# Kernel tuning notes

Hardware: AMD Instinct MI355X
Metric: run time of the kernel (lower is better)

Reference implementation:

```python
import jax, jax.numpy as jnp
import numpy as np

B, S, D = 4, 4096, 1024

def setup_inputs() -> dict:
    key = jax.random.key(0)
    k0, k1, k2, k3 = jax.random.split(key, 4)
    x = jax.random.normal(k0, (B, S, D), dtype=jnp.float32)
    # nn.Linear weights, applied as x @ W.T; init scaled ~1/sqrt(D)
    Wq = jax.random.normal(k1, (D, D), dtype=jnp.float32) / np.sqrt(D)
    Wk = jax.random.normal(k2, (D, D), dtype=jnp.float32) / np.sqrt(D)
    Wv = jax.random.normal(k3, (D, D), dtype=jnp.float32) / np.sqrt(D)
    return {"x": x, "Wq": Wq, "Wk": Wk, "Wv": Wv}

def reference(x, Wq, Wk, Wv):
    scale = x.shape[-1] ** (-0.5)
    Q = jnp.einsum('bsd,ed->bse', x, Wq)  # nn.Linear: x @ W.T
    K = jnp.einsum('bsd,ed->bse', x, Wk)
    V = jnp.einsum('bsd,ed->bse', x, Wv)
    scores = jax.nn.softmax(jnp.einsum('bqd,bkd->bqk', Q, K) * scale, axis=-1)
    return jnp.einsum('bqk,bkd->bqd', scores, V)
```

## Files before the change

### kernel.cpp

```cpp
#include <hip/hip_runtime.h>

typedef __bf16 bf16_t;
typedef bf16_t bf16x8 __attribute__((ext_vector_type(8)));
typedef float floatx4 __attribute__((ext_vector_type(4)));
typedef int i32x4 __attribute__((ext_vector_type(4)));

#define VMCNT(n) asm volatile("s_waitcnt vmcnt(" #n ")" ::: "memory")
#define LGKM(n)  asm volatile("s_waitcnt lgkmcnt(" #n ")" ::: "memory")
#define SCHED0   __builtin_amdgcn_sched_barrier(0)
#define DSR(dst, base, off) \
  asm volatile("ds_read_b128 %0, %1 offset:" #off : "=v"(dst) : "v"(base))

__device__ __forceinline__ void wg_barrier() {
  asm volatile("" ::: "memory");
  __builtin_amdgcn_s_barrier();
  asm volatile("" ::: "memory");
}

__device__ __forceinline__ void async_load16(const bf16_t* g, bf16_t* l) {
  __builtin_amdgcn_global_load_lds(
      (const __attribute__((address_space(1))) unsigned int*)g,
      (__attribute__((address_space(3))) unsigned int*)l, 16, 0, 0);
}

__device__ __forceinline__ unsigned lds_addr(const bf16_t* p) {
  return (unsigned)(unsigned long long)
      (__attribute__((address_space(3))) const bf16_t*)p;
}

__device__ __forceinline__ int xcd_swizzle(int p, int total) {
  return (total % 8 == 0) ? (p & 7) * (total >> 3) + (p >> 3) : p;
}

__device__ __forceinline__ void mfma16(
    floatx4 (&a4)[4][2],
    i32x4 x0, i32x4 x1, i32x4 x2, i32x4 x3,
    i32x4 x4, i32x4 x5, i32x4 x6, i32x4 x7,
    i32x4 y0, i32x4 y1, i32x4 y2, i32x4 y3)
{
  const bf16x8 A0[4] = {__builtin_bit_cast(bf16x8, x0), __builtin_bit_cast(bf16x8, x1),
                        __builtin_bit_cast(bf16x8, x2), __builtin_bit_cast(bf16x8, x3)};
  const bf16x8 A1[4] = {__builtin_bit_cast(bf16x8, x4), __builtin_bit_cast(bf16x8, x5),
                        __builtin_bit_cast(bf16x8, x6), __builtin_bit_cast(bf16x8, x7)};
  const bf16x8 B0[2] = {__builtin_bit_cast(bf16x8, y0), __builtin_bit_cast(bf16x8, y1)};
  const bf16x8 B1[2] = {__builtin_bit_cast(bf16x8, y2), __builtin_bit_cast(bf16x8, y3)};
  #pragma unroll
  for (int i = 0; i < 4; ++i)
    #pragma unroll
    for (int j = 0; j < 2; ++j) {
      a4[i][j] = __builtin_amdgcn_mfma_f32_16x16x32_bf16(A0[i], B0[j], a4[i][j], 0, 0, 0);
      a4[i][j] = __builtin_amdgcn_mfma_f32_16x16x32_bf16(A1[i], B1[j], a4[i][j], 0, 0, 0);
    }
}

__device__ __forceinline__ void gemm_acc256(
    const bf16_t* __restrict__ A, const bf16_t* __restrict__ B,
    int K, int lda, int ldb, int bm, int bn, floatx4 (&acc)[4][4][2])
{
  __shared__ bf16_t lA[2][16384];
  __shared__ bf16_t lB[2][16384];
  const int t = threadIdx.x;
  const int lane = t & 63;
  const int w = t >> 6;
  const int wm64 = (w & 1) * 64;
  const int wn32 = (w >> 1) * 32;
  const int fr = lane & 15;
  const int fk = ((lane >> 4) ^ ((fr >> 1) & 3)) * 8;

  const int r0 = t >> 2;
  const int ksw = ((t & 3) ^ ((r0 >> 1) & 3)) * 8;
  const long aRow = (long)(bm + r0) * lda + ksw;
  const long bRow = (long)(bn + r0) * ldb + ksw;
  const int NT = K >> 6;

  const unsigned baseA = lds_addr(&lA[0][0]);
  const unsigned baseB = lds_addr(&lB[0][0]);
  const unsigned fragA = baseA + (unsigned)(((wm64 + fr) * 32 + fk) * 2);
  const unsigned fragB = baseB + (unsigned)(((wn32 + fr) * 32 + fk) * 2);

  auto stageA = [&](int buf, int h, int u) {
    const bf16_t* s = A + aRow + (long)h * 128 * lda + u * 64;
    bf16_t* d = &lA[buf][h * 4096 + t * 8];
    async_load16(s, d);
    async_load16(s + 32, d + 8192);
  };
  auto stageB = [&](int buf, int h, int u) {
    const bf16_t* s = B + bRow + (long)h * 128 * ldb + u * 64;
    bf16_t* d = &lB[buf][h * 4096 + t * 8];
    async_load16(s, d);
    async_load16(s + 32, d + 8192);
  };

  stageA(0, 0, 0);
  stageB(0, 0, 0);
  stageB(0, 1, 0);
  stageA(0, 1, 0);
  stageA(1, 0, 1);
  stageB(1, 0, 1);
  VMCNT(8);
  wg_barrier();

  i32x4 al0,al1,al2,al3,al4,al5,al6,al7;
  i32x4 ah0,ah1,ah2,ah3,ah4,ah5,ah6,ah7;
  i32x4 vl0,vl1,vl2,vl3;
  i32x4 vh0,vh1,vh2,vh3;

  {
    const unsigned aC = fragA, bC = fragB;
    DSR(al0, aC, 0);     DSR(al1, aC, 1024);
    DSR(al2, aC, 2048);  DSR(al3, aC, 3072);
    DSR(al4, aC, 16384); DSR(al5, aC, 17408);
    DSR(al6, aC, 18432); DSR(al7, aC, 19456);
    DSR(vl0, bC, 0);     DSR(vl1, bC, 1024);
    DSR(vl2, bC, 16384); DSR(vl3, bC, 17408);
  }

  for (int u = 0; u < NT; ++u) {
    const int b = u & 1;
    const unsigned aC = fragA + (b ? 32768u : 0u);
    const unsigned bC = fragB + (b ? 32768u : 0u);
    const unsigned aN = fragA + (b ? 0u : 32768u);
    const unsigned bN = fragB + (b ? 0u : 32768u);

    if (u + 1 < NT) stageB(b ^ 1, 1, u + 1);
    if (u < NT - 1) { VMCNT(8); }
    DSR(vh0, bC, 8192);  DSR(vh1, bC, 9216);
    DSR(vh2, bC, 24576); DSR(vh3, bC, 25600);
    LGKM(4); SCHED0;
    __builtin_amdgcn_s_setprio(1);
    mfma16(acc[0], al0,al1,al2,al3,al4,al5,al6,al7, vl0,vl1,vl2,vl3);
    __builtin_amdgcn_s_setprio(0);
    wg_barrier();

    if (u + 1 < NT) stageA(b ^ 1, 1, u + 1);
    if (u < NT - 1) { VMCNT(8); }
    DSR(ah0, aC, 8192);  DSR(ah1, aC, 9216);
    DSR(ah2, aC, 10240); DSR(ah3, aC, 11264);
    DSR(ah4, aC, 24576); DSR(ah5, aC, 25600);
    DSR(ah6, aC, 26624); DSR(ah7, aC, 27648);
    LGKM(8); SCHED0;
    __builtin_amdgcn_s_setprio(1);
    mfma16(acc[1], al0,al1,al2,al3,al4,al5,al6,al7, vh0,vh1,vh2,vh3);
    __builtin_amdgcn_s_setprio(0);
    wg_barrier();

    if (u + 2 < NT) { stageA(b, 0, u + 2); VMCNT(8); }
    LGKM(0); SCHED0;
    __builtin_amdgcn_s_setprio(1);
    mfma16(acc[2], ah0,ah1,ah2,ah3,ah4,ah5,ah6,ah7, vl0,vl1,vl2,vl3);
    __builtin_amdgcn_s_setprio(0);
    wg_barrier();

    if (u + 2 < NT)       { stageB(b, 0, u + 2); VMCNT(8); }
    else if (u == NT - 2) { VMCNT(0); }
    if (u + 1 < NT) {
      DSR(al0, aN, 0);     DSR(al1, aN, 1024);
      DSR(al2, aN, 2048);  DSR(al3, aN, 3072);
      DSR(al4, aN, 16384); DSR(al5, aN, 17408);
      DSR(al6, aN, 18432); DSR(al7, aN, 19456);
      DSR(vl0, bN, 0);     DSR(vl1, bN, 1024);
      DSR(vl2, bN, 16384); DSR(vl3, bN, 17408);
    }
    __builtin_amdgcn_s_setprio(1);
    mfma16(acc[3], ah0,ah1,ah2,ah3,ah4,ah5,ah6,ah7, vh0,vh1,vh2,vh3);
    __builtin_amdgcn_s_setprio(0);
    wg_barrier();
  }
}

__device__ __forceinline__ void decode_grid(int& z, int& by, int& bx) {
  const int gx = gridDim.x, gy = gridDim.y;
  const int total = gx * gy * gridDim.z;
  int P = ((int)blockIdx.z * gy + (int)blockIdx.y) * gx + (int)blockIdx.x;
  int L = xcd_swizzle(P, total);
  z = L / (gx * gy);
  const int rem = L - z * gx * gy;
  if ((gx & 3) == 0 && (gy & 3) == 0) {
    const int sid = rem >> 4, w16 = rem & 15;
    const int spx = gx >> 2;
    const int sty = sid / spx, stx = sid - sty * spx;
    bx = stx * 4 + (w16 & 3);
    by = sty * 4 + (w16 >> 2);
  } else if ((gx & 3) == 0) {
    by = rem / gx; bx = rem - by * gx;
  } else {
    by = rem / gx; bx = rem - by * gx;
  }
}

__global__ __launch_bounds__(512, 2) void gemm_qkv(
    const bf16_t* __restrict__ xb, const bf16_t* __restrict__ Wqb,
    const bf16_t* __restrict__ Wkb, const bf16_t* __restrict__ Wvb,
    bf16_t* __restrict__ Q, bf16_t* __restrict__ Kp, bf16_t* __restrict__ Vt)
{
  const int L = xcd_swizzle((int)blockIdx.x, 768);
  const int z = L >> 8;
  const int r = L & 255;
  const bf16_t *A, *B; bf16_t* C;
  int bm, bn, ldc;
  if (z == 0)      { A = xb;  B = Wqb; C = Q;  bm = (r >> 2) * 256; bn = (r & 3) * 256; ldc = 1024; }
  else if (z == 1) { A = xb;  B = Wkb; C = Kp; bm = (r >> 2) * 256; bn = (r & 3) * 256; ldc = 1024; }
  else             { A = Wvb; B = xb;  C = Vt; bm = (r & 3) * 256; bn = (r >> 2) * 256; ldc = 16384; }
  floatx4 acc[4][4][2] = {};
  gemm_acc256(A, B, 1024, 1024, 1024, bm, bn, acc);

  const int t = threadIdx.x;
  const int lane = t & 63;
  const int w = t >> 6;
  const int wm64 = (w & 1) * 64;
  const int wn32 = (w >> 1) * 32;
  const int rq = (lane >> 4) * 4;
  const int c15 = lane & 15;
  #pragma unroll
  for (int q = 0; q < 4; ++q) {
    const int rB = bm + (q >> 1) * 128 + wm64;
    const int cB = bn + (q & 1) * 128 + wn32;
    #pragma unroll
    for (int i = 0; i < 4; ++i)
      #pragma unroll
      for (int j = 0; j < 2; ++j)
        #pragma unroll
        for (int r2 = 0; r2 < 4; ++r2)
          C[(long)(rB + i * 16 + rq + r2) * ldc + cB + j * 16 + c15] =
              (bf16_t)acc[q][i][j][r2];
  }
}

__global__ __launch_bounds__(512, 2) void gemm_qk_exp(
    const bf16_t* __restrict__ A, const bf16_t* __restrict__ B,
    bf16_t* __restrict__ C, float* __restrict__ rowsum,
    int K, int lda, int ldb, int ldc,
    long sA, long sB, long sC, long sR, float scale)
{
  __shared__ float rs[256];
  int z, by, bx;
  decode_grid(z, by, bx);
  A += (long)z * sA; B += (long)z * sB; C += (long)z * sC;
  rowsum += (long)z * sR;
  const int bm = by * 256, bn = bx * 256;
  if (threadIdx.x < 256) rs[threadIdx.x] = 0.f;
  floatx4 acc[4][4][2] = {};
  gemm_acc256(A, B, K, lda, ldb, bm, bn, acc);

  const int t = threadIdx.x;
  const int lane = t & 63;
  const int w = t >> 6;
  const int wm64 = (w & 1) * 64;
  const int wn32 = (w >> 1) * 32;
  const int rq = (lane >> 4) * 4;
  const int c15 = lane & 15;
  #pragma unroll
  for (int q = 0; q < 4; ++q) {
    const int rB = bm + (q >> 1) * 128 + wm64;
    const int cB = bn + (q & 1) * 128 + wn32;
    #pragma unroll
    for (int i = 0; i < 4; ++i) {
      #pragma unroll
      for (int r2 = 0; r2 < 4; ++r2) {
        const int row = rB + i * 16 + rq + r2;
        float psum = 0.f;
        #pragma unroll
        for (int j = 0; j < 2; ++j) {
          const float e = __expf(acc[q][i][j][r2] * scale);
          const bf16_t h = (bf16_t)e;
          C[(long)row * ldc + cB + j * 16 + c15] = h;
          psum += (float)h;
        }
        #pragma unroll
        for (int off = 8; off >= 1; off >>= 1)
          psum += __shfl_xor(psum, off, 16);
        if (c15 == 0) atomicAdd(&rs[row - bm], psum);
      }
    }
  }
  __syncthreads();
  if (t < 256) atomicAdd(&rowsum[bm + t], rs[t]);
}

__global__ __launch_bounds__(512, 2) void gemm_pv(
    const bf16_t* __restrict__ A, const bf16_t* __restrict__ B,
    float* __restrict__ C, const float* __restrict__ rowsum,
    int K, int lda, int ldb, int ldc,
    long sA, long sB, long sC, long sR)
{
  int z, by, bx;
  decode_grid(z, by, bx);
  A += (long)z * sA; B += (long)z * sB; C += (long)z * sC;
  rowsum += (long)z * sR;
  const int bm = by * 256, bn = bx * 256;
  floatx4 acc[4][4][2] = {};
  gemm_acc256(A, B, K, lda, ldb, bm, bn, acc);

  const int t = threadIdx.x;
  const int lane = t & 63;
  const int w = t >> 6;
  const int wm64 = (w & 1) * 64;
  const int wn32 = (w >> 1) * 32;
  const int rq = (lane >> 4) * 4;
  const int c15 = lane & 15;
  #pragma unroll
  for (int q = 0; q < 4; ++q) {
    const int rB = bm + (q >> 1) * 128 + wm64;
    const int cB = bn + (q & 1) * 128 + wn32;
    #pragma unroll
    for (int i = 0; i < 4; ++i) {
      #pragma unroll
      for (int r2 = 0; r2 < 4; ++r2) {
        const int row = rB + i * 16 + rq + r2;
        const float inv = 1.0f / rowsum[row];
        #pragma unroll
        for (int j = 0; j < 2; ++j)
          C[(long)row * ldc + cB + j * 16 + c15] = acc[q][i][j][r2] * inv;
      }
    }
  }
}

__global__ __launch_bounds__(256) void cvt_f32_bf16(
    const float* __restrict__ in, bf16_t* __restrict__ out, long n,
    float* __restrict__ rowsum, int nrs)
{
  const int bid = blockIdx.x;
  if (rowsum && bid < 64) {
    const int k = bid * 256 + threadIdx.x;
    if (k < nrs) rowsum[k] = 0.f;
  }
  long i = ((long)bid * 256 + threadIdx.x) * 4;
  if (i + 3 < n) {
    float4 f = *(const float4*)&in[i];
    bf16_t o[4] = {(bf16_t)f.x, (bf16_t)f.y, (bf16_t)f.z, (bf16_t)f.w};
    *(ulong1*)&out[i] = *(ulong1*)o;
  }
}

__global__ __launch_bounds__(256) void cvt3_f32_bf16(
    const float* __restrict__ w0, const float* __restrict__ w1,
    const float* __restrict__ w2, bf16_t* __restrict__ o0,
    bf16_t* __restrict__ o1, bf16_t* __restrict__ o2)
{
  const float* in = (blockIdx.z == 0) ? w0 : (blockIdx.z == 1) ? w1 : w2;
  bf16_t* out = (blockIdx.z == 0) ? o0 : (blockIdx.z == 1) ? o1 : o2;
  long i = ((long)blockIdx.x * 256 + threadIdx.x) * 4;
  float4 f = *(const float4*)&in[i];
  bf16_t o[4] = {(bf16_t)f.x, (bf16_t)f.y, (bf16_t)f.z, (bf16_t)f.w};
  *(ulong1*)&out[i] = *(ulong1*)o;
}

extern "C" void kernel_launch(void* const* d_in, const int* in_sizes, int n_in,
                              void* d_out, int out_size, void* d_ws, size_t ws_size,
                              hipStream_t stream) {
  (void)in_sizes; (void)n_in; (void)out_size;
  const float* x  = (const float*)d_in[0];
  const float* Wq = (const float*)d_in[1];
  const float* Wk = (const float*)d_in[2];
  const float* Wv = (const float*)d_in[3];
  float* out = (float*)d_out;

  const long BS = 16384, D = 1024, S = 4096;
  const long SD = S * D;
  const long SS = S * S;

  bf16_t* base = (bf16_t*)d_ws;
  bf16_t* Sc  = base;
  bf16_t* xb  = base;
  bf16_t* Wqb = base + SS;
  bf16_t* Wkb = Wqb + D * D;
  bf16_t* Wvb = Wkb + D * D;

  auto need = [&](long scElems) {
    return (size_t)(scElems + 3 * SS) * 2 + (size_t)BS * 4;
  };
  int nsc; long scE;
  if      (ws_size >= need(4 * SS)) { nsc = 4; scE = 4 * SS; }
  else if (ws_size >= need(2 * SS)) { nsc = 2; scE = 2 * SS; }
  else                              { nsc = 1; scE = SS + 3 * D * D; }

  bf16_t* Q  = base + scE;
  bf16_t* Kp = Q + SS;
  bf16_t* Vt = Kp + SS;
  float* rowsum = (float*)(Vt + SS);

  dim3 blk(256), blk512(512);
  cvt_f32_bf16<<<dim3((BS * D) / 1024), blk, 0, stream>>>(
      x, xb, BS * D, rowsum, (int)BS);
  cvt3_f32_bf16<<<dim3((D * D) / 1024, 1, 3), blk, 0, stream>>>(
      Wq, Wk, Wv, Wqb, Wkb, Wvb);

  gemm_qkv<<<dim3(768), blk512, 0, stream>>>(xb, Wqb, Wkb, Wvb, Q, Kp, Vt);

  const float scale = 0.03125f;
  if (nsc == 4) {
    gemm_qk_exp<<<dim3(16, 16, 4), blk512, 0, stream>>>(
        Q, Kp, Sc, rowsum, (int)D, (int)D, (int)D, (int)S,
        SD, SD, SS, S, scale);
    gemm_pv<<<dim3(4, 16, 4), blk512, 0, stream>>>(
        Sc, Vt, out, rowsum, (int)S, (int)S, (int)BS, (int)D,
        SS, S, SD, S);
  } else if (nsc == 2) {
    for (int p = 0; p < 2; ++p) {
      const long b0 = 2 * p;
      gemm_qk_exp<<<dim3(16, 16, 2), blk512, 0, stream>>>(
          Q + b0 * SD, Kp + b0 * SD, Sc, rowsum + b0 * S,
          (int)D, (int)D, (int)D, (int)S, SD, SD, SS, S, scale);
      gemm_pv<<<dim3(4, 16, 2), blk512, 0, stream>>>(
          Sc, Vt + b0 * S, out + b0 * SD, rowsum + b0 * S,
          (int)S, (int)S, (int)BS, (int)D, SS, S, SD, S);
    }
  } else {
    for (int b = 0; b < 4; ++b) {
      gemm_qk_exp<<<dim3(16, 16, 1), blk512, 0, stream>>>(
          Q + (long)b * SD, Kp + (long)b * SD, Sc, rowsum + (long)b * S,
          (int)D, (int)D, (int)D, (int)S, 0, 0, 0, 0, scale);
      gemm_pv<<<dim3(4, 16, 1), blk512, 0, stream>>>(
          Sc, Vt + (long)b * S, out + (long)b * SD, rowsum + (long)b * S,
          (int)S, (int)S, (int)BS, (int)D, 0, 0, 0, 0);
    }
  }
}
```

Measured before the change: 507.9 us.

## Restructure GEMM main loop into unrolled two-tile body with barrier-separated LDS reads

```diff
diff --git a/kernel.cpp b/kernel.cpp
--- a/kernel.cpp
+++ b/kernel.cpp
@@ -91,80 +91,68 @@
     async_load16(s + 32, d + 8192);
   };
 
+  i32x4 al0,al1,al2,al3,al4,al5,al6,al7;
+  i32x4 ah0,ah1,ah2,ah3,ah4,ah5,ah6,ah7;
+  i32x4 vl0,vl1,vl2,vl3;
+  i32x4 vh0,vh1,vh2,vh3;
+
+  auto tile_body = [&](int u, unsigned aC, unsigned bC) {
+    const int cb = u & 1, nb = cb ^ 1;
+    DSR(al0, aC, 0);     DSR(al1, aC, 1024);
+    DSR(al2, aC, 2048);  DSR(al3, aC, 3072);
+    DSR(al4, aC, 16384); DSR(al5, aC, 17408);
+    DSR(al6, aC, 18432); DSR(al7, aC, 19456);
+    DSR(vl0, bC, 0);     DSR(vl1, bC, 1024);
+    DSR(vl2, bC, 16384); DSR(vl3, bC, 17408);
+    if (u + 1 < NT) stageB(nb, 1, u + 1);
+    LGKM(8);
+    wg_barrier();
+    LGKM(0); SCHED0;
+    __builtin_amdgcn_s_setprio(1);
+    mfma16(acc[0], al0,al1,al2,al3,al4,al5,al6,al7, vl0,vl1,vl2,vl3);
+    __builtin_amdgcn_s_setprio(0);
+    wg_barrier();
+    DSR(vh0, bC, 8192);  DSR(vh1, bC, 9216);
+    DSR(vh2, bC, 24576); DSR(vh3, bC, 25600);
+    if (u + 1 < NT) stageA(nb, 1, u + 1);
+    wg_barrier();
+    LGKM(0); SCHED0;
+    __builtin_amdgcn_s_setprio(1);
+    mfma16(acc[1], al0,al1,al2,al3,al4,al5,al6,al7, vh0,vh1,vh2,vh3);
+    __builtin_amdgcn_s_setprio(0);
+    wg_barrier();
+    DSR(ah0, aC, 8192);  DSR(ah1, aC, 9216);
+    DSR(ah2, aC, 10240); DSR(ah3, aC, 11264);
+    DSR(ah4, aC, 24576); DSR(ah5, aC, 25600);
+    DSR(ah6, aC, 26624); DSR(ah7, aC, 27648);
+    if (u + 2 < NT) stageA(cb, 0, u + 2);
+    wg_barrier();
+    LGKM(0); SCHED0;
+    __builtin_amdgcn_s_setprio(1);
+    mfma16(acc[2], ah0,ah1,ah2,ah3,ah4,ah5,ah6,ah7, vl0,vl1,vl2,vl3);
+    __builtin_amdgcn_s_setprio(0);
+    wg_barrier();
+    if (u + 2 < NT)       { stageB(cb, 0, u + 2); VMCNT(4); }
+    else if (u == NT - 2) { VMCNT(0); }
+    wg_barrier();
+    __builtin_amdgcn_s_setprio(1);
+    mfma16(acc[3], ah0,ah1,ah2,ah3,ah4,ah5,ah6,ah7, vh0,vh1,vh2,vh3);
+    __builtin_amdgcn_s_setprio(0);
+    wg_barrier();
+  };
+
   stageA(0, 0, 0);
   stageB(0, 0, 0);
   stageB(0, 1, 0);
   stageA(0, 1, 0);
   stageA(1, 0, 1);
   stageB(1, 0, 1);
-  VMCNT(8);
+  VMCNT(4);
   wg_barrier();
 
-  i32x4 al0,al1,al2,al3,al4,al5,al6,al7;
-  i32x4 ah0,ah1,ah2,ah3,ah4,ah5,ah6,ah7;
-  i32x4 vl0,vl1,vl2,vl3;
-  i32x4 vh0,vh1,vh2,vh3;
-
-  {
-    const unsigned aC = fragA, bC = fragB;
-    DSR(al0, aC, 0);     DSR(al1, aC, 1024);
-    DSR(al2, aC, 2048);  DSR(al3, aC, 3072);
-    DSR(al4, aC, 16384); DSR(al5, aC, 17408);
-    DSR(al6, aC, 18432); DSR(al7, aC, 19456);
-    DSR(vl0, bC, 0);     DSR(vl1, bC, 1024);
-    DSR(vl2, bC, 16384); DSR(vl3, bC, 17408);
-  }
-
-  for (int u = 0; u < NT; ++u) {
-    const int b = u & 1;
-    const unsigned aC = fragA + (b ? 32768u : 0u);
-    const unsigned bC = fragB + (b ? 32768u : 0u);
-    const unsigned aN = fragA + (b ? 0u : 32768u);
-    const unsigned bN = fragB + (b ? 0u : 32768u);
-
-    if (u + 1 < NT) stageB(b ^ 1, 1, u + 1);
-    if (u < NT - 1) { VMCNT(8); }
-    DSR(vh0, bC, 8192);  DSR(vh1, bC, 9216);
-    DSR(vh2, bC, 24576); DSR(vh3, bC, 25600);
-    LGKM(4); SCHED0;
-    __builtin_amdgcn_s_setprio(1);
-    mfma16(acc[0], al0,al1,al2,al3,al4,al5,al6,al7, vl0,vl1,vl2,vl3);
-    __builtin_amdgcn_s_setprio(0);
-    wg_barrier();
-
-    if (u + 1 < NT) stageA(b ^ 1, 1, u + 1);
-    if (u < NT - 1) { VMCNT(8); }
-    DSR(ah0, aC, 8192);  DSR(ah1, aC, 9216);
-    DSR(ah2, aC, 10240); DSR(ah3, aC, 11264);
-    DSR(ah4, aC, 24576); DSR(ah5, aC, 25600);
-    DSR(ah6, aC, 26624); DSR(ah7, aC, 27648);
-    LGKM(8); SCHED0;
-    __builtin_amdgcn_s_setprio(1);
-    mfma16(acc[1], al0,al1,al2,al3,al4,al5,al6,al7, vh0,vh1,vh2,vh3);
-    __builtin_amdgcn_s_setprio(0);
-    wg_barrier();
-
-    if (u + 2 < NT) { stageA(b, 0, u + 2); VMCNT(8); }
-    LGKM(0); SCHED0;
-    __builtin_amdgcn_s_setprio(1);
-    mfma16(acc[2], ah0,ah1,ah2,ah3,ah4,ah5,ah6,ah7, vl0,vl1,vl2,vl3);
-    __builtin_amdgcn_s_setprio(0);
-    wg_barrier();
-
-    if (u + 2 < NT)       { stageB(b, 0, u + 2); VMCNT(8); }
-    else if (u == NT - 2) { VMCNT(0); }
-    if (u + 1 < NT) {
-      DSR(al0, aN, 0);     DSR(al1, aN, 1024);
-      DSR(al2, aN, 2048);  DSR(al3, aN, 3072);
-      DSR(al4, aN, 16384); DSR(al5, aN, 17408);
-      DSR(al6, aN, 18432); DSR(al7, aN, 19456);
-      DSR(vl0, bN, 0);     DSR(vl1, bN, 1024);
-      DSR(vl2, bN, 16384); DSR(vl3, bN, 17408);
-    }
-    __builtin_amdgcn_s_setprio(1);
-    mfma16(acc[3], ah0,ah1,ah2,ah3,ah4,ah5,ah6,ah7, vh0,vh1,vh2,vh3);
-    __builtin_amdgcn_s_setprio(0);
-    wg_barrier();
+  for (int u = 0; u < NT; u += 2) {
+    tile_body(u,     fragA,          fragB);
+    tile_body(u + 1, fragA + 32768u, fragB + 32768u);
   }
 }
 
@@ -181,8 +169,6 @@
     const int sty = sid / spx, stx = sid - sty * spx;
     bx = stx * 4 + (w16 & 3);
     by = sty * 4 + (w16 >> 2);
-  } else if ((gx & 3) == 0) {
-    by = rem / gx; bx = rem - by * gx;
   } else {
     by = rem / gx; bx = rem - by * gx;
   }
```

Result: faster. 493.2 us, median of 2 (-2.9%).
